# Performance work log

Measured on AMD Instinct MI355X. Metric: run time of the kernel, lower is better.

## Reference

```python
import jax, jax.numpy as jnp
import numpy as np

N_NODES = 50000
NEG_SLOPE = 0.2


def gat_layer(x, src, dst, W, a_src, a_dst, b, concat):
    # x: [N, Fin]; W: [Fin, H*C]; a_src/a_dst: [H, C]; b: [H*C] or [C]
    H, C = a_src.shape
    h = (x @ W).reshape(-1, H, C)                      # [N, H, C]
    al_s = jnp.einsum('nhc,hc->nh', h, a_src)          # [N, H]
    al_d = jnp.einsum('nhc,hc->nh', h, a_dst)          # [N, H]
    e = jax.nn.leaky_relu(al_s[src] + al_d[dst], NEG_SLOPE)   # [E, H]
    # segment softmax over incoming edges of each destination node
    e_max = jax.ops.segment_max(e, dst, num_segments=N_NODES)  # [N, H]
    ex = jnp.exp(e - e_max[dst])
    denom = jax.ops.segment_sum(ex, dst, num_segments=N_NODES)
    alpha = ex / (denom[dst] + 1e-16)                  # [E, H]
    msg = h[src] * alpha[:, :, None]                   # [E, H, C]
    out = jax.ops.segment_sum(msg, dst, num_segments=N_NODES)  # [N, H, C]
    out = out.reshape(N_NODES, H * C) if concat else out.mean(axis=1)
    return out + b


def setup_inputs() -> dict:
    key = jax.random.key(0)
    ks = jax.random.split(key, 16)
    x = jax.random.normal(ks[0], (N_NODES, 12), dtype=jnp.float32)
    edge_index = jax.random.randint(ks[1], (2, 400000), 0, N_NODES, dtype=jnp.int32)
    H, C = 8, 64
    s = 0.1
    W1 = jax.random.normal(ks[2], (12, H * C), jnp.float32) * s
    as1 = jax.random.normal(ks[3], (H, C), jnp.float32) * s
    ad1 = jax.random.normal(ks[4], (H, C), jnp.float32) * s
    b1 = jnp.zeros((H * C,), jnp.float32)
    W2 = jax.random.normal(ks[5], (H * C, H * C), jnp.float32) * s
    as2 = jax.random.normal(ks[6], (H, C), jnp.float32) * s
    ad2 = jax.random.normal(ks[7], (H, C), jnp.float32) * s
    b2 = jnp.zeros((H * C,), jnp.float32)
    W3 = jax.random.normal(ks[8], (H * C, H * 5), jnp.float32) * s
    as3 = jax.random.normal(ks[9], (H, 5), jnp.float32) * s
    ad3 = jax.random.normal(ks[10], (H, 5), jnp.float32) * s
    b3 = jnp.zeros((5,), jnp.float32)
    return {"x": x, "edge_index": edge_index,
            "W1": W1, "as1": as1, "ad1": ad1, "b1": b1,
            "W2": W2, "as2": as2, "ad2": ad2, "b2": b2,
            "W3": W3, "as3": as3, "ad3": ad3, "b3": b3}


def reference(x, edge_index, W1, as1, ad1, b1, W2, as2, ad2, b2, W3, as3, ad3, b3):
    # add self-loops (PyG GATConv default add_self_loops=True)
    loop = jnp.arange(N_NODES, dtype=edge_index.dtype)
    src = jnp.concatenate([edge_index[0], loop])
    dst = jnp.concatenate([edge_index[1], loop])
    h = gat_layer(x, src, dst, W1, as1, ad1, b1, concat=True)
    h = jax.nn.relu(h)
    h = gat_layer(h, src, dst, W2, as2, ad2, b2, concat=True)
    h = jax.nn.relu(h)
    h = gat_layer(h, src, dst, W3, as3, ad3, b3, concat=False)
    return jax.nn.log_softmax(h, axis=1)
```

## Files before the change

### kernel.cpp

```cpp
#include <hip/hip_runtime.h>
#include <hip/hip_bf16.h>

#define NN    50000
#define MP    50048
#define E0C   400000
#define ETOT  450000
#define HH    8
#define FF    512
#define F3    40
#define C3    5
#define MAXE  128
#define NBLK  ((NN + 1023) / 1024)
#define MT2   (MP / 128)
#define GT2   (MT2 * 4)

typedef __attribute__((ext_vector_type(8))) short bf16x8;
typedef __attribute__((ext_vector_type(8))) short s16x8;
typedef __attribute__((ext_vector_type(4))) float f32x4;

__device__ inline unsigned short f2bf(float f) {
    union { float f; unsigned int u; } v; v.f = f;
    unsigned int r = v.u + 0x7FFF + ((v.u >> 16) & 1);
    return (unsigned short)(r >> 16);
}
__device__ inline float bf2f(unsigned short u) {
    union { unsigned int i; float f; } v; v.i = ((unsigned int)u) << 16;
    return v.f;
}

__global__ void count_kernel(const int* __restrict__ ei, int* __restrict__ cnt) {
    int e = blockIdx.x * blockDim.x + threadIdx.x;
    if (e >= ETOT) return;
    int dst = (e < E0C) ? ei[E0C + e] : (e - E0C);
    atomicAdd(&cnt[dst], 1);
}

__global__ __launch_bounds__(1024) void scan_blocks(const int* __restrict__ cnt,
                                                    int* __restrict__ offs,
                                                    int* __restrict__ bsum) {
    __shared__ int s[1024];
    int tid = threadIdx.x;
    int i = blockIdx.x * 1024 + tid;
    s[tid] = (i < NN) ? cnt[i] : 0;
    __syncthreads();
    for (int d = 1; d < 1024; d <<= 1) {
        int add = (tid >= d) ? s[tid - d] : 0;
        __syncthreads();
        s[tid] += add;
        __syncthreads();
    }
    if (i < NN) offs[i + 1] = s[tid];
    if (tid == 1023) bsum[blockIdx.x] = s[1023];
}

__global__ __launch_bounds__(1024) void scan_add(int* __restrict__ offs,
                                                 const int* __restrict__ bsum) {
    __shared__ int pref;
    int tid = threadIdx.x;
    if (tid < 64) {
        int v = (tid < blockIdx.x) ? bsum[tid] : 0;
#pragma unroll
        for (int d = 32; d; d >>= 1) v += __shfl_xor(v, d);
        if (tid == 0) pref = v;
    }
    __syncthreads();
    int i = blockIdx.x * 1024 + tid;
    if (i < NN) offs[i + 1] += pref;
    if (i == 0) offs[0] = 0;
}

__global__ void scatter_kernel(const int* __restrict__ ei, const int* __restrict__ offs,
                               int* __restrict__ cur, int* __restrict__ srcs) {
    int e = blockIdx.x * blockDim.x + threadIdx.x;
    if (e >= ETOT) return;
    int src, dst;
    if (e < E0C) { src = ei[e]; dst = ei[E0C + e]; }
    else         { src = dst = e - E0C; }
    int pos = offs[dst] + atomicAdd(&cur[dst], 1);
    srcs[pos] = src;
}

__global__ void prep_all(const float* __restrict__ W2, const float* __restrict__ W3,
                         unsigned short* __restrict__ W2T, unsigned short* __restrict__ W3T,
                         unsigned short* __restrict__ A2) {
    int i = blockIdx.x * blockDim.x + threadIdx.x;
    if (i < FF * FF) {
        int n = i >> 9, k = i & 511;
        W2T[i] = f2bf(W2[k * FF + n]);
        return;
    }
    int j = i - FF * FF;
    if (j < 48 * 512) {
        int n = j >> 9, k = j & 511;
        W3T[j] = (n < F3) ? f2bf(W3[k * F3 + n]) : 0;
        return;
    }
    int l = j - 48 * 512;
    if (l < (MP - NN) * FF) A2[(size_t)NN * FF + l] = 0;
}

__global__ __launch_bounds__(256) void gemm1_fused(
    const float* __restrict__ x, const float* __restrict__ W1,
    const float* __restrict__ as1, const float* __restrict__ ad1,
    unsigned short* __restrict__ hb, float* __restrict__ al_s,
    float* __restrict__ al_d) {
    __shared__ float xs[64 * 12];
    int t = threadIdx.x;
    int n0 = blockIdx.x * 64;
    int nvalid = NN - n0; if (nvalid > 64) nvalid = 64;

    for (int j = t; j < nvalid * 12; j += 256) xs[j] = x[(size_t)n0 * 12 + j];
    __syncthreads();

    int f = t * 2;
    float w0[12], w1[12];
#pragma unroll
    for (int k = 0; k < 12; ++k) {
        float2 wv = *(const float2*)&W1[k * FF + f];
        w0[k] = wv.x; w1[k] = wv.y;
    }
    float2 asv = *(const float2*)&as1[f];
    float2 adv = *(const float2*)&ad1[f];
    int head = t >> 5;

    for (int ni = 0; ni < nvalid; ++ni) {
        const float* xp = &xs[ni * 12];
        float4 xa = *(const float4*)xp;
        float4 xb = *(const float4*)(xp + 4);
        float4 xc = *(const float4*)(xp + 8);
        float xv[12] = {xa.x, xa.y, xa.z, xa.w, xb.x, xb.y, xb.z, xb.w,
                        xc.x, xc.y, xc.z, xc.w};
        float h0 = 0.f, h1 = 0.f;
#pragma unroll
        for (int k = 0; k < 12; ++k) { h0 += xv[k] * w0[k]; h1 += xv[k] * w1[k]; }
        unsigned int u = ((unsigned int)f2bf(h1) << 16) | f2bf(h0);
        *(unsigned int*)&hb[(size_t)(n0 + ni) * FF + f] = u;
        float ps = h0 * asv.x + h1 * asv.y;
        float pd = h0 * adv.x + h1 * adv.y;
#pragma unroll
        for (int d = 1; d < 32; d <<= 1) {
            ps += __shfl_xor(ps, d);
            pd += __shfl_xor(pd, d);
        }
        if ((t & 31) == 0) {
            al_s[(size_t)(n0 + ni) * HH + head] = ps;
            al_d[(size_t)(n0 + ni) * HH + head] = pd;
        }
    }
}

__global__ __launch_bounds__(256) void attn_gather(
    const unsigned short* __restrict__ Hb,
    const float* __restrict__ alS, const float* __restrict__ alD,
    const int* __restrict__ offs, const int* __restrict__ srcs,
    const float* __restrict__ bias,
    float* __restrict__ out_f32, unsigned short* __restrict__ out_b16, int relu) {
    __shared__ float alpha_sh[4][MAXE][HH];
    __shared__ int   srcs_sh[4][MAXE];
    int w = threadIdx.x >> 6, lane = threadIdx.x & 63;
    int n = blockIdx.x * 4 + w;
    if (n >= NN) return;
    int h = lane >> 3, es = lane & 7;
    int beg = offs[n], end = offs[n + 1], deg = end - beg;

    float ald = alD[n * HH + h];
    float m = -1e30f, den = 0.f, idn;

    if (deg <= MAXE) {
        for (int e = es; e < deg; e += 8) {
            int s = srcs[beg + e];
            if (h == 0) srcs_sh[w][e] = s;
            float sc = alS[s * HH + h] + ald;
            sc = sc > 0.f ? sc : 0.2f * sc;
            alpha_sh[w][e][h] = sc;
            m = fmaxf(m, sc);
        }
        m = fmaxf(m, __shfl_xor(m, 1));
        m = fmaxf(m, __shfl_xor(m, 2));
        m = fmaxf(m, __shfl_xor(m, 4));
        for (int e = es; e < deg; e += 8) {
            float ex = __expf(alpha_sh[w][e][h] - m);
            den += ex;
            alpha_sh[w][e][h] = ex;
        }
        den += __shfl_xor(den, 1);
        den += __shfl_xor(den, 2);
        den += __shfl_xor(den, 4);
        idn = 1.f / (den + 1e-16f);
    } else {
        for (int e = es; e < deg; e += 8) {
            int s = srcs[beg + e];
            float sc = alS[s * HH + h] + ald;
            sc = sc > 0.f ? sc : 0.2f * sc;
            m = fmaxf(m, sc);
        }
        m = fmaxf(m, __shfl_xor(m, 1));
        m = fmaxf(m, __shfl_xor(m, 2));
        m = fmaxf(m, __shfl_xor(m, 4));
        for (int e = es; e < deg; e += 8) {
            int s = srcs[beg + e];
            float sc = alS[s * HH + h] + ald;
            sc = sc > 0.f ? sc : 0.2f * sc;
            den += __expf(sc - m);
        }
        den += __shfl_xor(den, 1);
        den += __shfl_xor(den, 2);
        den += __shfl_xor(den, 4);
        idn = 1.f / (den + 1e-16f);
    }

    int f0 = lane * 8;
    float acc[8] = {};
    if (deg <= MAXE) {
        int e = 0;
        for (; e + 4 <= deg; e += 4) {
            int s0 = srcs_sh[w][e + 0], s1 = srcs_sh[w][e + 1];
            int s2 = srcs_sh[w][e + 2], s3 = srcs_sh[w][e + 3];
            bf16x8 v0 = *(const bf16x8*)&Hb[(size_t)s0 * FF + f0];
            bf16x8 v1 = *(const bf16x8*)&Hb[(size_t)s1 * FF + f0];
            bf16x8 v2 = *(const bf16x8*)&Hb[(size_t)s2 * FF + f0];
            bf16x8 v3 = *(const bf16x8*)&Hb[(size_t)s3 * FF + f0];
            float a0 = alpha_sh[w][e + 0][h], a1 = alpha_sh[w][e + 1][h];
            float a2 = alpha_sh[w][e + 2][h], a3 = alpha_sh[w][e + 3][h];
#pragma unroll
            for (int k = 0; k < 8; ++k) {
                acc[k] += a0 * bf2f((unsigned short)v0[k]);
                acc[k] += a1 * bf2f((unsigned short)v1[k]);
                acc[k] += a2 * bf2f((unsigned short)v2[k]);
                acc[k] += a3 * bf2f((unsigned short)v3[k]);
            }
        }
        for (; e < deg; ++e) {
            int s = srcs_sh[w][e];
            float a = alpha_sh[w][e][h];
            bf16x8 v = *(const bf16x8*)&Hb[(size_t)s * FF + f0];
#pragma unroll
            for (int k = 0; k < 8; ++k)
                acc[k] += a * bf2f((unsigned short)v[k]);
        }
#pragma unroll
        for (int k = 0; k < 8; ++k) acc[k] *= idn;
    } else {
        for (int e = 0; e < deg; ++e) {
            int s = srcs[beg + e];
            float sc = alS[s * HH + h] + ald;
            sc = sc > 0.f ? sc : 0.2f * sc;
            float a = __expf(sc - m) * idn;
            bf16x8 v = *(const bf16x8*)&Hb[(size_t)s * FF + f0];
#pragma unroll
            for (int k = 0; k < 8; ++k)
                acc[k] += a * bf2f((unsigned short)v[k]);
        }
    }
    float4 b0 = *(const float4*)&bias[f0];
    float4 b1 = *(const float4*)&bias[f0 + 4];
    float bv[8] = {b0.x, b0.y, b0.z, b0.w, b1.x, b1.y, b1.z, b1.w};
    float vv[8];
#pragma unroll
    for (int k = 0; k < 8; ++k) {
        float t = acc[k] + bv[k];
        vv[k] = relu ? fmaxf(t, 0.f) : t;
    }
    if (out_f32) {
        float4 o0 = {vv[0], vv[1], vv[2], vv[3]};
        float4 o1 = {vv[4], vv[5], vv[6], vv[7]};
        *(float4*)&out_f32[(size_t)n * FF + f0] = o0;
        *(float4*)&out_f32[(size_t)n * FF + f0 + 4] = o1;
    }
    if (out_b16) {
        s16x8 ov;
#pragma unroll
        for (int k = 0; k < 8; ++k) ov[k] = (short)f2bf(vv[k]);
        *(s16x8*)&out_b16[(size_t)n * FF + f0] = ov;
    }
}

__global__ __launch_bounds__(256) void gemm_mfma(
    const unsigned short* __restrict__ A,
    const unsigned short* __restrict__ BT,
    const float* __restrict__ a_s, const float* __restrict__ a_d,
    unsigned short* __restrict__ Cb,
    float* __restrict__ alS, float* __restrict__ alD,
    int N, int K) {
    __shared__ unsigned short As[128 * 64];
    __shared__ unsigned short Bs[128 * 64];
    int t = threadIdx.x;
    int wave = t >> 6, lane = t & 63;
    int wr = wave >> 1, wc = wave & 1;

    int bid = blockIdx.x;
    int mt, nt;
    if (bid < (MT2 / 8) * 32) {
        int g = bid >> 5, r = bid & 31;
        mt = g * 8 + (r & 7);
        nt = r >> 3;
    } else {
        int t2 = bid - (MT2 / 8) * 32;
        mt = (MT2 / 8) * 8 + (t2 >> 2);
        nt = t2 & 3;
    }
    int m0 = mt * 128, n0 = nt * 128;

    f32x4 acc[4][4] = {};
    int kg = lane >> 4;
    int lr = lane & 15;

    for (int k0 = 0; k0 < K; k0 += 64) {
#pragma unroll
        for (int q = 0; q < 4; ++q) {
            int c   = q * 256 + t;
            int row = c >> 3, kc = c & 7;
            int kcs = kc ^ (row & 7);
            const unsigned short* ga = A + (size_t)(m0 + row) * K + k0 + kcs * 8;
            const unsigned short* gb = BT + (size_t)(n0 + row) * K + k0 + kcs * 8;
            unsigned short* la = As + (size_t)(q * 256 + wave * 64) * 8;
            unsigned short* lb = Bs + (size_t)(q * 256 + wave * 64) * 8;
            __builtin_amdgcn_global_load_lds(
                (const __attribute__((address_space(1))) void*)ga,
                (__attribute__((address_space(3))) void*)la, 16, 0, 0);
            __builtin_amdgcn_global_load_lds(
                (const __attribute__((address_space(1))) void*)gb,
                (__attribute__((address_space(3))) void*)lb, 16, 0, 0);
        }
        __syncthreads();
#pragma unroll
        for (int ks = 0; ks < 2; ++ks) {
            bf16x8 af[4], bf[4];
#pragma unroll
            for (int i = 0; i < 4; ++i) {
                int rowa = wr * 64 + i * 16 + lr;
                af[i] = *(const bf16x8*)&As[rowa * 64 + (((ks << 2) | kg) ^ (rowa & 7)) * 8];
                int rowb = wc * 64 + i * 16 + lr;
                bf[i] = *(const bf16x8*)&Bs[rowb * 64 + (((ks << 2) | kg) ^ (rowb & 7)) * 8];
            }
#pragma unroll
            for (int i = 0; i < 4; ++i)
#pragma unroll
                for (int j = 0; j < 4; ++j)
                    acc[i][j] = __builtin_amdgcn_mfma_f32_16x16x32_bf16(
                        af[i], bf[j], acc[i][j], 0, 0, 0);
        }
        __syncthreads();
    }

    int head = (n0 >> 6) + wc;
    float asv[4], adv[4];
#pragma unroll
    for (int j = 0; j < 4; ++j) {
        int cc = n0 + wc * 64 + j * 16 + lr;
        asv[j] = a_s[cc];
        adv[j] = a_d[cc];
    }
#pragma unroll
    for (int i = 0; i < 4; ++i) {
#pragma unroll
        for (int reg = 0; reg < 4; ++reg) {
            float ps = 0.f, pd = 0.f;
#pragma unroll
            for (int j = 0; j < 4; ++j) {
                ps += acc[i][j][reg] * asv[j];
                pd += acc[i][j][reg] * adv[j];
            }
#pragma unroll
            for (int d = 1; d < 16; d <<= 1) {
                ps += __shfl_xor(ps, d);
                pd += __shfl_xor(pd, d);
            }
            if (lr == 0) {
                int r = m0 + wr * 64 + i * 16 + kg * 4 + reg;
                alS[(size_t)r * HH + head] = ps;
                alD[(size_t)r * HH + head] = pd;
            }
        }
    }

#pragma unroll
    for (int i = 0; i < 4; ++i) {
        int rb = m0 + wr * 64 + i * 16 + kg * 4;
#pragma unroll
        for (int j = 0; j < 4; ++j) {
            int cc = n0 + wc * 64 + j * 16 + lr;
#pragma unroll
            for (int reg = 0; reg < 4; ++reg)
                Cb[(size_t)(rb + reg) * N + cc] = f2bf(acc[i][j][reg]);
        }
    }
}

__global__ __launch_bounds__(256) void gemm3_mfma(
    const unsigned short* __restrict__ A,
    const unsigned short* __restrict__ BT,
    float* __restrict__ C) {
    __shared__ unsigned short As[128 * 64];
    __shared__ unsigned short Bs[48 * 64];
    int t = threadIdx.x;
    int wave = t >> 6, lane = t & 63;
    int m0 = blockIdx.x * 128;
    int kg = lane >> 4, lr = lane & 15;

    f32x4 acc[2][3] = {};

    for (int k0 = 0; k0 < 512; k0 += 64) {
#pragma unroll
        for (int q = 0; q < 4; ++q) {
            int c   = q * 256 + t;
            int row = c >> 3, kc = c & 7;
            int kcs = kc ^ (row & 7);
            const unsigned short* ga = A + (size_t)(m0 + row) * 512 + k0 + kcs * 8;
            unsigned short* la = &As[(size_t)(q * 256 + wave * 64) * 8];
            __builtin_amdgcn_global_load_lds(
                (const __attribute__((address_space(1))) void*)ga,
                (__attribute__((address_space(3))) void*)la, 16, 0, 0);
        }
        {
            int c   = t;
            int row = c >> 3, kc = c & 7;
            int kcs = kc ^ (row & 7);
            const unsigned short* gb = BT + (size_t)row * 512 + k0 + kcs * 8;
            unsigned short* lb = &Bs[(size_t)(wave * 64) * 8];
            __builtin_amdgcn_global_load_lds(
                (const __attribute__((address_space(1))) void*)gb,
                (__attribute__((address_space(3))) void*)lb, 16, 0, 0);
        }
        if (t < 128) {
            int c   = 256 + t;
            int row = c >> 3, kc = c & 7;
            int kcs = kc ^ (row & 7);
            const unsigned short* gb = BT + (size_t)row * 512 + k0 + kcs * 8;
            unsigned short* lb = &Bs[(size_t)(256 + wave * 64) * 8];
            __builtin_amdgcn_global_load_lds(
                (const __attribute__((address_space(1))) void*)gb,
                (__attribute__((address_space(3))) void*)lb, 16, 0, 0);
        }
        __syncthreads();
#pragma unroll
        for (int ks = 0; ks < 2; ++ks) {
            bf16x8 af[2], bf[3];
#pragma unroll
            for (int i = 0; i < 2; ++i) {
                int rowa = wave * 32 + i * 16 + lr;
                af[i] = *(const bf16x8*)&As[rowa * 64 + (((ks << 2) | kg) ^ (rowa & 7)) * 8];
            }
#pragma unroll
            for (int j = 0; j < 3; ++j) {
                int rowb = j * 16 + lr;
                bf[j] = *(const bf16x8*)&Bs[rowb * 64 + (((ks << 2) | kg) ^ (rowb & 7)) * 8];
            }
#pragma unroll
            for (int i = 0; i < 2; ++i)
#pragma unroll
                for (int j = 0; j < 3; ++j)
                    acc[i][j] = __builtin_amdgcn_mfma_f32_16x16x32_bf16(
                        af[i], bf[j], acc[i][j], 0, 0, 0);
        }
        __syncthreads();
    }

#pragma unroll
    for (int i = 0; i < 2; ++i) {
        int rb = m0 + wave * 32 + i * 16 + kg * 4;
#pragma unroll
        for (int j = 0; j < 3; ++j) {
            int cc = j * 16 + lr;
            if (cc >= F3) continue;
#pragma unroll
            for (int reg = 0; reg < 4; ++reg) {
                int r = rb + reg;
                if (r < NN) C[(size_t)r * F3 + cc] = acc[i][j][reg];
            }
        }
    }
}

__global__ void al40_kernel(const float* __restrict__ h3, const float* __restrict__ as3,
                            const float* __restrict__ ad3, float* __restrict__ al_s,
                            float* __restrict__ al_d) {
    int n = blockIdx.x * blockDim.x + threadIdx.x;
    if (n >= NN) return;
#pragma unroll
    for (int hh = 0; hh < HH; ++hh) {
        float s = 0.f, d = 0.f;
#pragma unroll
        for (int c = 0; c < C3; ++c) {
            float v = h3[(size_t)n * F3 + hh * C3 + c];
            s += v * as3[hh * C3 + c];
            d += v * ad3[hh * C3 + c];
        }
        al_s[n * HH + hh] = s;
        al_d[n * HH + hh] = d;
    }
}

__global__ __launch_bounds__(256) void attn3_kernel(
    const float* __restrict__ h3, const float* __restrict__ al_s,
    const float* __restrict__ al_d, const int* __restrict__ offs,
    const int* __restrict__ srcs, const float* __restrict__ b3,
    float* __restrict__ out) {
    __shared__ float alpha_sh[4][MAXE][HH];
    __shared__ int   srcs_sh[4][MAXE];
    __shared__ float idn_sh[4][HH], m_sh[4][HH], ald_sh2[4][HH];
    __shared__ float accs[4][F3];
    __shared__ float vv[4][C3];
    int w = threadIdx.x >> 6, lane = threadIdx.x & 63;
    int n = blockIdx.x * 4 + w;
    int h = lane >> 3, es = lane & 7;
    int beg = offs[n], end = offs[n + 1], deg = end - beg;

    float ald = al_d[n * HH + h];
    float m = -1e30f, den = 0.f, idn;
    if (deg <= MAXE) {
        for (int e = es; e < deg; e += 8) {
            int s = srcs[beg + e];
            if (h == 0) srcs_sh[w][e] = s;
            float sc = al_s[s * HH + h] + ald;
            sc = sc > 0.f ? sc : 0.2f * sc;
            alpha_sh[w][e][h] = sc;
            m = fmaxf(m, sc);
        }
        m = fmaxf(m, __shfl_xor(m, 1));
        m = fmaxf(m, __shfl_xor(m, 2));
        m = fmaxf(m, __shfl_xor(m, 4));
        for (int e = es; e < deg; e += 8) {
            float ex = __expf(alpha_sh[w][e][h] - m);
            den += ex;
            alpha_sh[w][e][h] = ex;
        }
        den += __shfl_xor(den, 1);
        den += __shfl_xor(den, 2);
        den += __shfl_xor(den, 4);
        idn = 1.f / (den + 1e-16f);
        if (es == 0) idn_sh[w][h] = idn;
    } else {
        for (int e = es; e < deg; e += 8) {
            int s = srcs[beg + e];
            float sc = al_s[s * HH + h] + ald;
            sc = sc > 0.f ? sc : 0.2f * sc;
            m = fmaxf(m, sc);
        }
        m = fmaxf(m, __shfl_xor(m, 1));
        m = fmaxf(m, __shfl_xor(m, 2));
        m = fmaxf(m, __shfl_xor(m, 4));
        for (int e = es; e < deg; e += 8) {
            int s = srcs[beg + e];
            float sc = al_s[s * HH + h] + ald;
            sc = sc > 0.f ? sc : 0.2f * sc;
            den += __expf(sc - m);
        }
        den += __shfl_xor(den, 1);
        den += __shfl_xor(den, 2);
        den += __shfl_xor(den, 4);
        idn = 1.f / (den + 1e-16f);
        if (es == 0) { idn_sh[w][h] = idn; m_sh[w][h] = m; ald_sh2[w][h] = ald; }
    }
    __syncthreads();

    if (lane < F3) {
        int hh = lane / C3;
        float acc = 0.f;
        if (deg <= MAXE) {
            int e = 0;
            for (; e + 4 <= deg; e += 4) {
                int s0 = srcs_sh[w][e + 0], s1 = srcs_sh[w][e + 1];
                int s2 = srcs_sh[w][e + 2], s3 = srcs_sh[w][e + 3];
                float v0 = h3[(size_t)s0 * F3 + lane];
                float v1 = h3[(size_t)s1 * F3 + lane];
                float v2 = h3[(size_t)s2 * F3 + lane];
                float v3 = h3[(size_t)s3 * F3 + lane];
                acc += alpha_sh[w][e + 0][hh] * v0 + alpha_sh[w][e + 1][hh] * v1
                     + alpha_sh[w][e + 2][hh] * v2 + alpha_sh[w][e + 3][hh] * v3;
            }
            for (; e < deg; ++e) {
                int s = srcs_sh[w][e];
                acc += alpha_sh[w][e][hh] * h3[(size_t)s * F3 + lane];
            }
        } else {
            float mm = m_sh[w][hh], aald = ald_sh2[w][hh];
            for (int e = 0; e < deg; ++e) {
                int s = srcs[beg + e];
                float sc = al_s[s * HH + hh] + aald;
                sc = sc > 0.f ? sc : 0.2f * sc;
                acc += __expf(sc - mm) * h3[(size_t)s * F3 + lane];
            }
        }
        accs[w][lane] = acc * idn_sh[w][hh];
    }
    __syncthreads();
    if (lane < C3) {
        float s = 0.f;
#pragma unroll
        for (int hh = 0; hh < HH; ++hh) s += accs[w][hh * C3 + lane];
        vv[w][lane] = s * 0.125f + b3[lane];
    }
    __syncthreads();
    if (lane < C3) {
        float mx = vv[w][0];
#pragma unroll
        for (int c = 1; c < C3; ++c) mx = fmaxf(mx, vv[w][c]);
        float se = 0.f;
#pragma unroll
        for (int c = 0; c < C3; ++c) se += __expf(vv[w][c] - mx);
        out[(size_t)n * C3 + lane] = vv[w][lane] - mx - logf(se);
    }
}

extern "C" void kernel_launch(void* const* d_in, const int* in_sizes, int n_in,
                              void* d_out, int out_size, void* d_ws, size_t ws_size,
                              hipStream_t stream) {
    const float* x   = (const float*)d_in[0];
    const int*   ei  = (const int*)d_in[1];
    const float* W1  = (const float*)d_in[2];
    const float* as1 = (const float*)d_in[3];
    const float* ad1 = (const float*)d_in[4];
    const float* b1  = (const float*)d_in[5];
    const float* W2  = (const float*)d_in[6];
    const float* as2 = (const float*)d_in[7];
    const float* ad2 = (const float*)d_in[8];
    const float* b2  = (const float*)d_in[9];
    const float* W3  = (const float*)d_in[10];
    const float* as3 = (const float*)d_in[11];
    const float* ad3 = (const float*)d_in[12];
    const float* b3  = (const float*)d_in[13];
    float* out = (float*)d_out;

    auto au = [](size_t v) { return (v + 255) & ~(size_t)255; };
    char* p = (char*)d_ws;
    size_t szHb = au((size_t)MP * FF * 2);
    char* r1 = p;
    unsigned short* Hb1 = (unsigned short*)r1;
    unsigned short* Hb2 = (unsigned short*)r1;
    p += szHb;
    char* r2 = p;
    unsigned short* A2   = (unsigned short*)r2;
    unsigned short* Bb16 = (unsigned short*)r2;
    unsigned short* W2T  = (unsigned short*)(r2 + szHb);
    p = r2 + szHb + au((size_t)FF * FF * 2);
    unsigned short* W3T = (unsigned short*)p;  p += au((size_t)48 * 512 * 2);
    float* alS  = (float*)p;  p += au((size_t)MP * HH * 4);
    float* alD  = (float*)p;  p += au((size_t)MP * HH * 4);
    float* h3   = (float*)p;  p += au((size_t)NN * F3 * 4);
    int* offs   = (int*)p;    p += au((size_t)(NN + 1) * 4);
    int* cnt    = (int*)p;    p += au((size_t)NN * 4);
    int* srcs   = (int*)p;    p += au((size_t)ETOT * 4);
    int* bsum   = (int*)p;    p += au(64 * 4);

    hipMemsetAsync(cnt, 0, (size_t)NN * 4, stream);
    count_kernel<<<(ETOT + 255) / 256, 256, 0, stream>>>(ei, cnt);
    scan_blocks<<<NBLK, 1024, 0, stream>>>(cnt, offs, bsum);
    scan_add<<<NBLK, 1024, 0, stream>>>(offs, bsum);
    hipMemsetAsync(cnt, 0, (size_t)NN * 4, stream);
    scatter_kernel<<<(ETOT + 255) / 256, 256, 0, stream>>>(ei, offs, cnt, srcs);
    {
        int prep_elems = FF * FF + 48 * 512 + (MP - NN) * FF;
        prep_all<<<(prep_elems + 255) / 256, 256, 0, stream>>>(W2, W3, W2T, W3T, A2);
    }

    gemm1_fused<<<(NN + 63) / 64, 256, 0, stream>>>(x, W1, as1, ad1, Hb1, alS, alD);
    attn_gather<<<(NN + 3) / 4, 256, 0, stream>>>(Hb1, alS, alD, offs, srcs, b1,
                                                  nullptr, A2, 1);

    gemm_mfma<<<GT2, 256, 0, stream>>>(
        A2, W2T, as2, ad2, Hb2, alS, alD, FF, FF);
    attn_gather<<<(NN + 3) / 4, 256, 0, stream>>>(Hb2, alS, alD, offs, srcs, b2,
                                                  nullptr, Bb16, 1);

    gemm3_mfma<<<MP / 128, 256, 0, stream>>>(Bb16, W3T, h3);
    al40_kernel<<<(NN + 255) / 256, 256, 0, stream>>>(h3, as3, ad3, alS, alD);
    attn3_kernel<<<NN / 4, 256, 0, stream>>>(h3, alS, alD, offs, srcs, b3, out);
}
```

Before: 356.5 us.

## Double-buffer GEMM LDS tiles and fold counter reset into scan kernel

The layer-2 MFMA GEMM now uses two LDS buffers per operand and issues the async global-to-LDS loads for the next K tile before computing on the current one. This is meant to overlap memory latency with MFMA work. It doubles LDS use to 64 KB per block, which may lower occupancy. Separately, scan_blocks zeroes the count array after reading it, which removes one hipMemsetAsync launch before the scatter kernel.

```diff
diff --git a/kernel.cpp b/kernel.cpp
--- a/kernel.cpp
+++ b/kernel.cpp
@@ -35,13 +35,15 @@
     atomicAdd(&cnt[dst], 1);
 }
 
-__global__ __launch_bounds__(1024) void scan_blocks(const int* __restrict__ cnt,
+__global__ __launch_bounds__(1024) void scan_blocks(int* __restrict__ cnt,
                                                     int* __restrict__ offs,
                                                     int* __restrict__ bsum) {
     __shared__ int s[1024];
     int tid = threadIdx.x;
     int i = blockIdx.x * 1024 + tid;
-    s[tid] = (i < NN) ? cnt[i] : 0;
+    int v = (i < NN) ? cnt[i] : 0;
+    if (i < NN) cnt[i] = 0;
+    s[tid] = v;
     __syncthreads();
     for (int d = 1; d < 1024; d <<= 1) {
         int add = (tid >= d) ? s[tid - d] : 0;
@@ -282,8 +284,8 @@
     unsigned short* __restrict__ Cb,
     float* __restrict__ alS, float* __restrict__ alD,
     int N, int K) {
-    __shared__ unsigned short As[128 * 64];
-    __shared__ unsigned short Bs[128 * 64];
+    __shared__ unsigned short As[2][128 * 64];
+    __shared__ unsigned short Bs[2][128 * 64];
     int t = threadIdx.x;
     int wave = t >> 6, lane = t & 63;
     int wr = wave >> 1, wc = wave & 1;
@@ -305,7 +307,7 @@
     int kg = lane >> 4;
     int lr = lane & 15;
 
-    for (int k0 = 0; k0 < K; k0 += 64) {
+    auto STAGE = [&](int buf, int k0) {
 #pragma unroll
         for (int q = 0; q < 4; ++q) {
             int c   = q * 256 + t;
@@ -313,8 +315,8 @@
             int kcs = kc ^ (row & 7);
             const unsigned short* ga = A + (size_t)(m0 + row) * K + k0 + kcs * 8;
             const unsigned short* gb = BT + (size_t)(n0 + row) * K + k0 + kcs * 8;
-            unsigned short* la = As + (size_t)(q * 256 + wave * 64) * 8;
-            unsigned short* lb = Bs + (size_t)(q * 256 + wave * 64) * 8;
+            unsigned short* la = &As[buf][(size_t)(q * 256 + wave * 64) * 8];
+            unsigned short* lb = &Bs[buf][(size_t)(q * 256 + wave * 64) * 8];
             __builtin_amdgcn_global_load_lds(
                 (const __attribute__((address_space(1))) void*)ga,
                 (__attribute__((address_space(3))) void*)la, 16, 0, 0);
@@ -322,16 +324,25 @@
                 (const __attribute__((address_space(1))) void*)gb,
                 (__attribute__((address_space(3))) void*)lb, 16, 0, 0);
         }
-        __syncthreads();
+    };
+
+    const int NT = K / 64;
+    STAGE(0, 0);
+    __syncthreads();
+    int cur = 0;
+    for (int kt = 0; kt < NT; ++kt) {
+        if (kt + 1 < NT) STAGE(cur ^ 1, (kt + 1) * 64);
+        const unsigned short* Ac = As[cur];
+        const unsigned short* Bc = Bs[cur];
 #pragma unroll
         for (int ks = 0; ks < 2; ++ks) {
             bf16x8 af[4], bf[4];
 #pragma unroll
             for (int i = 0; i < 4; ++i) {
                 int rowa = wr * 64 + i * 16 + lr;
-                af[i] = *(const bf16x8*)&As[rowa * 64 + (((ks << 2) | kg) ^ (rowa & 7)) * 8];
+                af[i] = *(const bf16x8*)&Ac[rowa * 64 + (((ks << 2) | kg) ^ (rowa & 7)) * 8];
                 int rowb = wc * 64 + i * 16 + lr;
-                bf[i] = *(const bf16x8*)&Bs[rowb * 64 + (((ks << 2) | kg) ^ (rowb & 7)) * 8];
+                bf[i] = *(const bf16x8*)&Bc[rowb * 64 + (((ks << 2) | kg) ^ (rowb & 7)) * 8];
             }
 #pragma unroll
             for (int i = 0; i < 4; ++i)
@@ -341,6 +352,7 @@
                         af[i], bf[j], acc[i][j], 0, 0, 0);
         }
         __syncthreads();
+        cur ^= 1;
     }
 
     int head = (n0 >> 6) + wc;
@@ -647,7 +659,6 @@
     count_kernel<<<(ETOT + 255) / 256, 256, 0, stream>>>(ei, cnt);
     scan_blocks<<<NBLK, 1024, 0, stream>>>(cnt, offs, bsum);
     scan_add<<<NBLK, 1024, 0, stream>>>(offs, bsum);
-    hipMemsetAsync(cnt, 0, (size_t)NN * 4, stream);
     scatter_kernel<<<(ETOT + 255) / 256, 256, 0, stream>>>(ei, offs, cnt, srcs);
     {
         int prep_elems = FF * FF + 48 * 512 + (MP - NN) * FF;
```

New measurement: 344.8 us. 1.03x faster.
